# Optimization experiments

Hardware: AMD Instinct MI355X
Metric: run time of the kernel (lower is better)

The kernel has to match this reference:

```python
import jax, jax.numpy as jnp
import numpy as np
from jax import lax

EPS = 1e-5

# --- ApproxSign (ReActNet binary activation, STE with polynomial grad) ---
@jax.custom_vjp
def approx_sign(x):
    return jnp.sign(x)

def _as_fwd(x):
    return jnp.sign(x), x

def _as_bwd(x, g):
    # d/dx of piecewise-polynomial approx: 2-2|x| for |x|<1, else 0
    return (g * jnp.maximum(0.0, 2.0 - 2.0 * jnp.abs(x)),)

approx_sign.defvjp(_as_fwd, _as_bwd)


def rsign(x, bias):
    # learnable per-channel shift then binarize
    return approx_sign(x + bias[None, :, None, None])


def scaled_sign_weight(w):
    # per-output-channel scale * sign(w); straight-through identity grad to w
    scale = jnp.mean(jnp.abs(w), axis=(1, 2, 3), keepdims=True)
    bw = scale * jnp.sign(w)
    return lax.stop_gradient(bw - w) + w


def conv(x, w, stride, pad):
    return lax.conv_general_dilated(
        x, w, window_strides=(stride, stride), padding=[(pad, pad), (pad, pad)],
        dimension_numbers=("NCHW", "OIHW", "NCHW"))


def bn(x, g, b, m, v):
    inv = g / jnp.sqrt(v + EPS)
    return x * inv[None, :, None, None] + (b - m * inv)[None, :, None, None]


def rprelu(x, gamma, beta, zeta):
    t = x - gamma[None, :, None, None]
    return jnp.where(t > 0, t, beta[None, :, None, None] * t) + zeta[None, :, None, None]


def avgpool2(x):
    B, C, H, W = x.shape
    return x.reshape(B, C, H // 2, 2, W // 2, 2).mean(axis=(3, 5))


def setup_inputs() -> dict:
    key = jax.random.key(0)
    ks = jax.random.split(key, 16)
    C = 256
    d = {}
    d["x"] = jax.random.normal(ks[0], (64, C, 28, 28), dtype=jnp.float32)
    d["rsign_bias"] = jax.random.normal(ks[1], (C,), dtype=jnp.float32) * 0.1
    d["w1"] = jax.random.normal(ks[2], (C, C, 3, 3), dtype=jnp.float32) * 0.05
    d["bn1_g"] = jnp.ones((C,), jnp.float32)
    d["bn1_b"] = jnp.zeros((C,), jnp.float32)
    d["bn1_m"] = jax.random.normal(ks[3], (C,), dtype=jnp.float32) * 0.1
    d["bn1_v"] = jax.random.uniform(ks[4], (C,), dtype=jnp.float32, minval=0.5, maxval=1.5)
    d["w21"] = jax.random.normal(ks[5], (C, C, 1, 1), dtype=jnp.float32) * 0.05
    d["bn21_g"] = jnp.ones((C,), jnp.float32)
    d["bn21_b"] = jnp.zeros((C,), jnp.float32)
    d["bn21_m"] = jax.random.normal(ks[6], (C,), dtype=jnp.float32) * 0.1
    d["bn21_v"] = jax.random.uniform(ks[7], (C,), dtype=jnp.float32, minval=0.5, maxval=1.5)
    d["w22"] = jax.random.normal(ks[8], (C, C, 1, 1), dtype=jnp.float32) * 0.05
    d["bn22_g"] = jnp.ones((C,), jnp.float32)
    d["bn22_b"] = jnp.zeros((C,), jnp.float32)
    d["bn22_m"] = jax.random.normal(ks[9], (C,), dtype=jnp.float32) * 0.1
    d["bn22_v"] = jax.random.uniform(ks[10], (C,), dtype=jnp.float32, minval=0.5, maxval=1.5)
    d["pr_gamma"] = jax.random.normal(ks[11], (C,), dtype=jnp.float32) * 0.1
    d["pr_beta"] = jnp.full((C,), 0.25, jnp.float32)
    d["pr_zeta"] = jax.random.normal(ks[12], (C,), dtype=jnp.float32) * 0.1
    return d


def reference(x, rsign_bias, w1, bn1_g, bn1_b, bn1_m, bn1_v,
              w21, bn21_g, bn21_b, bn21_m, bn21_v,
              w22, bn22_g, bn22_b, bn22_m, bn22_v,
              pr_gamma, pr_beta, pr_zeta):
    # layer1: RSign -> 3x3 stride2 binary conv -> BN
    out = bn(conv(rsign(x, rsign_bias), scaled_sign_weight(w1), 2, 1),
             bn1_g, bn1_b, bn1_m, bn1_v)
    out1 = out + avgpool2(x)                       # residual with avgpooled input
    out2 = rprelu(out1, pr_gamma, pr_beta, pr_zeta)
    # two parallel 1x1 binary conv branches (shared RSign bias)
    a = rsign(out2, rsign_bias)
    out2_1 = bn(conv(a, scaled_sign_weight(w21), 1, 0), bn21_g, bn21_b, bn21_m, bn21_v)
    out2_2 = bn(conv(a, scaled_sign_weight(w22), 1, 0), bn22_g, bn22_b, bn22_m, bn22_v)
    out4_1 = rprelu(out2_1 + out2, pr_gamma, pr_beta, pr_zeta)
    out4_2 = rprelu(out2_2 + out2, pr_gamma, pr_beta, pr_zeta)
    return jnp.concatenate([out4_1, out4_2], axis=1)  # [B, 2C, H/2, W/2]
```

## Files before the change

kernel.cpp:

```cpp
#include <hip/hip_runtime.h>
#include <stdint.h>

#define EPS_BN 1e-5f

#define C 256
#define H 28
#define W 28
#define R196 196
#define M_TOT 12544
#define K1 2304

typedef __attribute__((ext_vector_type(4))) int   i32x4;
typedef __attribute__((ext_vector_type(4))) float f32x4;
typedef unsigned short ushort_t;
typedef unsigned int uint_t;

__device__ __forceinline__ char sgn_i8(float v) {
    return v > 0.f ? (char)1 : (v < 0.f ? (char)-1 : (char)0);
}
__device__ __forceinline__ uint_t sgn_b(float v) {
    return (uint_t)(unsigned char)sgn_i8(v);
}

__device__ __forceinline__ void gload16(const void* g, void* l) {
    __builtin_amdgcn_global_load_lds(
        (const __attribute__((address_space(1))) void*)g,
        (__attribute__((address_space(3))) void*)l, 16, 0, 0);
}


__global__ __launch_bounds__(256) void prep_sign(
    const float* __restrict__ w1,
    const float* __restrict__ bn1_g, const float* __restrict__ bn1_b,
    const float* __restrict__ bn1_m, const float* __restrict__ bn1_v,
    const float* __restrict__ w21,
    const float* __restrict__ bn21_g, const float* __restrict__ bn21_b,
    const float* __restrict__ bn21_m, const float* __restrict__ bn21_v,
    const float* __restrict__ w22,
    const float* __restrict__ bn22_g, const float* __restrict__ bn22_b,
    const float* __restrict__ bn22_m, const float* __restrict__ bn22_v,
    const float* __restrict__ x, const float* __restrict__ bias,
    char* __restrict__ bw1, char* __restrict__ bw2,
    float* __restrict__ alpha1, float* __restrict__ beta1,
    float* __restrict__ alpha2, float* __restrict__ beta2,
    char* __restrict__ a1p, float* __restrict__ pool)
{
    __shared__ uint_t lsign[1792];
    float* red = (float*)lsign;
    const int bid = blockIdx.x;
    const int t = threadIdx.x;

    if (bid < 768) {
        if (bid < 256) {
            const int oc = bid;
            const float* w = w1 + oc * K1;
            float s = 0.f;
            for (int i = t; i < K1; i += 256) s += fabsf(w[i]);
            red[t] = s; __syncthreads();
            for (int o = 128; o > 0; o >>= 1) {
                if (t < o) red[t] += red[t + o];
                __syncthreads();
            }
            const float scale = red[0] * (1.f / (float)K1);
            if (t == 0) {
                const float inv = bn1_g[oc] * rsqrtf(bn1_v[oc] + EPS_BN);
                alpha1[oc] = scale * inv;
                beta1[oc]  = bn1_b[oc] - bn1_m[oc] * inv;
            }
            const int ic = ((t & 3) << 6) | (t >> 2);
#pragma unroll
            for (int tap = 0; tap < 9; ++tap)
                bw1[oc * K1 + tap * 256 + t] = sgn_i8(w[ic * 9 + tap]);
        } else {
            const bool br2 = (bid >= 512);
            const int oc = (bid - 256) & 255;
            const float* w = (br2 ? w22 : w21) + oc * 256;
            red[t] = fabsf(w[t]); __syncthreads();
            for (int o = 128; o > 0; o >>= 1) {
                if (t < o) red[t] += red[t + o];
                __syncthreads();
            }
            const float scale = red[0] * (1.f / 256.f);
            const int n = oc + (br2 ? 256 : 0);
            if (t == 0) {
                const float g = br2 ? bn22_g[oc] : bn21_g[oc];
                const float b = br2 ? bn22_b[oc] : bn21_b[oc];
                const float m = br2 ? bn22_m[oc] : bn21_m[oc];
                const float v = br2 ? bn22_v[oc] : bn21_v[oc];
                const float inv = g * rsqrtf(v + EPS_BN);
                alpha2[n] = scale * inv;
                beta2[n]  = b - m * inv;
            }
            bw2[n * 256 + t] = sgn_i8(w[t]);
        }
        return;
    }

    const int sb = bid - 768;
    const int hh = sb & 1;
    const int bo = sb >> 1;
    const int b = bo / 14, oh = bo % 14;
    const float* xb = x + (size_t)(b * 256) * 784 + (2 * oh) * 28;

    for (int i = t; i < 896; i += 256) {
        const int lc = i / 7, q = i - lc * 7;
        const int c = 64 * (lc >> 5) + 32 * hh + (lc & 31);
        const float bc = bias[c];
        const float4 v0 = *(const float4*)(xb + c * 784 + 4 * q);
        const float4 v1 = *(const float4*)(xb + c * 784 + 28 + 4 * q);
        uint_t s0 = sgn_b(v0.x + bc) | (sgn_b(v0.y + bc) << 8) |
                    (sgn_b(v0.z + bc) << 16) | (sgn_b(v0.w + bc) << 24);
        uint_t s1 = sgn_b(v1.x + bc) | (sgn_b(v1.y + bc) << 8) |
                    (sgn_b(v1.z + bc) << 16) | (sgn_b(v1.w + bc) << 24);
        lsign[lc * 7 + q] = s0;
        lsign[896 + lc * 7 + q] = s1;
        float2 pr;
        pr.x = 0.25f * (v0.x + v0.y + v1.x + v1.y);
        pr.y = 0.25f * (v0.z + v0.w + v1.z + v1.w);
        *(float2*)(pool + (size_t)(b * 256 + c) * 196 + oh * 14 + 2 * q) = pr;
    }
    __syncthreads();

    for (int i = t; i < 448; i += 256) {
        const int tl = i & 31;
        const int q = (i >> 5) % 7;
        const int row = i / 224;
        const int tt = 32 * hh + tl;
        uint_t d[4];
#pragma unroll
        for (int e = 0; e < 4; ++e)
            d[e] = lsign[row * 896 + (tl + 32 * e) * 7 + q];
        char* orow = a1p + (size_t)((b * 30 + 2 * oh + row + 1) * 30) * 256;
#pragma unroll
        for (int j = 0; j < 4; ++j) {
            uint_t o = ((d[0] >> (8 * j)) & 0xffu)
                     | (((d[1] >> (8 * j)) & 0xffu) << 8)
                     | (((d[2] >> (8 * j)) & 0xffu) << 16)
                     | (((d[3] >> (8 * j)) & 0xffu) << 24);
            *(uint_t*)(orow + (4 * q + j + 1) * 256 + 4 * tt) = o;
        }
    }

    {
        char* orow0 = a1p + (size_t)((b * 30 + 2 * oh + 1) * 30) * 256;
        char* orow1 = a1p + (size_t)((b * 30 + 2 * oh + 2) * 30) * 256;
        const int bo2 = 128 * hh + (t & 127);
        if (t < 128) { orow0[bo2] = 0; orow1[bo2] = 0; }
        else         { orow0[29 * 256 + bo2] = 0; orow1[29 * 256 + bo2] = 0; }
    }
    if (oh == 0) {
        char* r0  = a1p + (size_t)(b * 900) * 256;
        char* r29 = a1p + (size_t)(b * 900 + 29 * 30) * 256;
        for (int idx = t; idx < 30 * 128; idx += 256) {
            const int colo = (idx >> 7) * 256 + 128 * hh + (idx & 127);
            r0[colo] = 0; r29[colo] = 0;
        }
    }
}

__global__ __launch_bounds__(512) void conv1_i8(
    const char* __restrict__ a1p,
    const char* __restrict__ bw1,
    const float* __restrict__ alpha1, const float* __restrict__ beta1,
    const float* __restrict__ p,
    const float* __restrict__ rsb,
    const float* __restrict__ prg, const float* __restrict__ prb,
    const float* __restrict__ prz,
    float* __restrict__ out2,
    char* __restrict__ a2)
{
    __shared__ char lA[2][64 * 128];
    __shared__ char lB[2][64 * 128];

    const int bid = blockIdx.x;
    const int wgid = (bid & 7) * 98 + (bid >> 3);
    const int mtile = wgid >> 2;
    const int ntile = wgid & 3;

    const int tid = threadIdx.x;
    const int wave = tid >> 6;
    const int lane = tid & 63;
    const int col = lane & 15;
    const int krow = lane >> 4;
    const int wr = wave >> 2;
    const int wc = wave & 3;
    const int l8 = lane >> 3;
    const int s8 = lane & 7;
    const int swz = ((s8 ^ l8) << 4);

    int pbA;
    {
        const int grow = wave * 8 + l8;
        const int m = mtile * 64 + grow;
        const int b = m / 196, r = m % 196;
        const int oh = r / 14, ow = r % 14;
        pbA = ((b * 30 + 2 * oh) * 30 + 2 * ow) * 256 + swz;
    }
    const int pbB = (ntile * 64 + wave * 8 + l8) * K1 + swz;

    int rswz[2];
#pragma unroll
    for (int ks = 0; ks < 2; ++ks)
        rswz[ks] = ((ks * 4 + krow) ^ (col & 7)) << 4;

    i32x4 acc[2] = {};

    auto stage = [&](int step, int buf) {
        const int tap = step >> 1;
        const int kc0 = (step & 1) << 7;
        const int kh = tap / 3, kw = tap - kh * 3;
        const int aoff = (kh * 30 + kw) * 256 + kc0;
        gload16(a1p + pbA + aoff, &lA[buf][0] + wave * 1024);
        gload16(bw1 + pbB + step * 128, &lB[buf][0] + wave * 1024);
    };

    stage(0, 0);

    int cur = 0;
    for (int step = 0; step < 18; ++step) {
        if (step + 1 < 18) {
            stage(step + 1, cur ^ 1);
            asm volatile("s_waitcnt vmcnt(2)" ::: "memory");
        } else {
            asm volatile("s_waitcnt vmcnt(0)" ::: "memory");
        }
        __builtin_amdgcn_s_barrier();
        __builtin_amdgcn_sched_barrier(0);

#pragma unroll
        for (int ks = 0; ks < 2; ++ks) {
            i32x4 bf[2], af;
#pragma unroll
            for (int im = 0; im < 2; ++im) {
                const int row = wr * 32 + im * 16 + col;
                bf[im] = *(const i32x4*)(&lA[cur][0] + row * 128 + rswz[ks]);
            }
            {
                const int row = wc * 16 + col;
                af = *(const i32x4*)(&lB[cur][0] + row * 128 + rswz[ks]);
            }
#pragma unroll
            for (int im = 0; im < 2; ++im)
                acc[im] = __builtin_amdgcn_mfma_i32_16x16x64_i8(
                    af, bf[im], acc[im], 0, 0, 0);
        }
        __builtin_amdgcn_sched_barrier(0);
        __builtin_amdgcn_s_barrier();
        cur ^= 1;
    }

#pragma unroll
    for (int im = 0; im < 2; ++im) {
        const int m = mtile * 64 + wr * 32 + im * 16 + col;
        const int b = m / 196, r = m % 196;
        const int n0 = ntile * 64 + wc * 16 + krow * 4;
        char spack[4];
#pragma unroll
        for (int j = 0; j < 4; ++j) {
            const int n = n0 + j;
            const int idx = (b * 256 + n) * 196 + r;
            float v = alpha1[n] * (float)acc[im][j] + beta1[n] + p[idx];
            const float t = v - prg[n];
            const float o = (t > 0.f ? t : prb[n] * t) + prz[n];
            out2[idx] = o;
            spack[j] = sgn_i8(o + rsb[n]);
        }
        *(char4*)(a2 + m * 256 + n0) = *(char4*)spack;
    }
}

__global__ __launch_bounds__(512) void conv1x1_i8(
    const char* __restrict__ a2,
    const char* __restrict__ bw2,
    const float* __restrict__ alpha2, const float* __restrict__ beta2,
    const float* __restrict__ out2,
    const float* __restrict__ prg, const float* __restrict__ prb,
    const float* __restrict__ prz,
    float* __restrict__ out)
{
    __shared__ char lA[2][64 * 128];
    __shared__ char lB[2][64 * 128];

    const int bid = blockIdx.x;
    const int wgid = (bid & 7) * 196 + (bid >> 3);
    const int mtile = wgid >> 3;
    const int ntile = wgid & 7;

    const int tid = threadIdx.x;
    const int wave = tid >> 6;
    const int lane = tid & 63;
    const int col = lane & 15;
    const int krow = lane >> 4;
    const int wr = wave >> 2;
    const int wc = wave & 3;
    const int l8 = lane >> 3;
    const int s8 = lane & 7;
    const int swz = ((s8 ^ l8) << 4);

    const int pbA = (mtile * 64 + wave * 8 + l8) * 256 + swz;
    const int pbB = (ntile * 64 + wave * 8 + l8) * 256 + swz;

#pragma unroll
    for (int h = 0; h < 2; ++h) {
        gload16(a2 + pbA + h * 128, &lA[h][0] + wave * 1024);
        gload16(bw2 + pbB + h * 128, &lB[h][0] + wave * 1024);
    }
    asm volatile("s_waitcnt vmcnt(0)" ::: "memory");
    __builtin_amdgcn_s_barrier();
    __builtin_amdgcn_sched_barrier(0);

    i32x4 acc[2] = {};
#pragma unroll
    for (int ks = 0; ks < 4; ++ks) {
        const int h = ks >> 1, k2 = ks & 1;
        const int ro = ((k2 * 4 + krow) ^ (col & 7)) << 4;
        i32x4 bf[2], af;
#pragma unroll
        for (int im = 0; im < 2; ++im) {
            const int row = wr * 32 + im * 16 + col;
            bf[im] = *(const i32x4*)(&lA[h][0] + row * 128 + ro);
        }
        {
            const int row = wc * 16 + col;
            af = *(const i32x4*)(&lB[h][0] + row * 128 + ro);
        }
#pragma unroll
        for (int im = 0; im < 2; ++im)
            acc[im] = __builtin_amdgcn_mfma_i32_16x16x64_i8(
                af, bf[im], acc[im], 0, 0, 0);
    }

#pragma unroll
    for (int im = 0; im < 2; ++im) {
        const int m = mtile * 64 + wr * 32 + im * 16 + col;
        const int b = m / 196, r = m % 196;
#pragma unroll
        for (int j = 0; j < 4; ++j) {
            const int n = ntile * 64 + wc * 16 + krow * 4 + j;
            const int oc = n & 255;
            float v = alpha2[n] * (float)acc[im][j] + beta2[n]
                    + out2[(b * 256 + oc) * 196 + r];
            const float t = v - prg[oc];
            out[(size_t)(b * 512 + n) * 196 + r] =
                (t > 0.f ? t : prb[oc] * t) + prz[oc];
        }
    }
}

extern "C" void kernel_launch(void* const* d_in, const int* in_sizes, int n_in,
                              void* d_out, int out_size, void* d_ws, size_t ws_size,
                              hipStream_t stream)
{
    (void)in_sizes; (void)n_in; (void)out_size; (void)ws_size;

    const float* x         = (const float*)d_in[0];
    const float* rsign_b   = (const float*)d_in[1];
    const float* w1        = (const float*)d_in[2];
    const float* bn1_g     = (const float*)d_in[3];
    const float* bn1_b     = (const float*)d_in[4];
    const float* bn1_m     = (const float*)d_in[5];
    const float* bn1_v     = (const float*)d_in[6];
    const float* w21       = (const float*)d_in[7];
    const float* bn21_g    = (const float*)d_in[8];
    const float* bn21_b    = (const float*)d_in[9];
    const float* bn21_m    = (const float*)d_in[10];
    const float* bn21_v    = (const float*)d_in[11];
    const float* w22       = (const float*)d_in[12];
    const float* bn22_g    = (const float*)d_in[13];
    const float* bn22_b    = (const float*)d_in[14];
    const float* bn22_m    = (const float*)d_in[15];
    const float* bn22_v    = (const float*)d_in[16];
    const float* pr_gamma  = (const float*)d_in[17];
    const float* pr_beta   = (const float*)d_in[18];
    const float* pr_zeta   = (const float*)d_in[19];

    char* ws = (char*)d_ws;
    size_t off = 0;
    char* a1p     = (char*)(ws + off);  off += (size_t)14745600;
    char* bw1     = (char*)(ws + off);  off += (size_t)589824;
    char* bw2     = (char*)(ws + off);  off += (size_t)131072;
    float* pool   = (float*)(ws + off); off += (size_t)3211264 * 4;
    float* out2   = (float*)(ws + off); off += (size_t)3211264 * 4;
    char* a2      = (char*)(ws + off);  off += (size_t)3211264;
    float* alpha1 = (float*)(ws + off); off += 1024;
    float* beta1  = (float*)(ws + off); off += 1024;
    float* alpha2 = (float*)(ws + off); off += 2048;
    float* beta2  = (float*)(ws + off); off += 2048;

    prep_sign<<<2560, 256, 0, stream>>>(
        w1, bn1_g, bn1_b, bn1_m, bn1_v,
        w21, bn21_g, bn21_b, bn21_m, bn21_v,
        w22, bn22_g, bn22_b, bn22_m, bn22_v,
        x, rsign_b,
        bw1, bw2, alpha1, beta1, alpha2, beta2, a1p, pool);

    conv1_i8<<<784, 512, 0, stream>>>(
        a1p, bw1, alpha1, beta1, pool, rsign_b,
        pr_gamma, pr_beta, pr_zeta, out2, a2);

    conv1x1_i8<<<1568, 512, 0, stream>>>(
        a2, bw2, alpha2, beta2, out2,
        pr_gamma, pr_beta, pr_zeta, (float*)d_out);
}
```

Measured before the change: 60.92 us.

## Enlarge conv workgroup tiles to 128x128 with 1024-thread blocks

Both int8 MFMA conv kernels move from 64x64 to 128x128 output tiles, using 16 waves per block. Each wave now computes a 2x2 set of 16x16 MFMA tiles instead of 2x1, and the LDS buffers double in size. The XCD-aware block remapping is replaced by a plain mtile/ntile split. The goal is more operand reuse and fewer global loads per output. The cost is fewer blocks (196 and 392) on a GPU with many CUs, which risks leaving CUs idle, plus higher LDS and register use per block.

```diff
diff --git a/kernel.cpp b/kernel.cpp
--- a/kernel.cpp
+++ b/kernel.cpp
@@ -158,7 +158,7 @@
     }
 }
 
-__global__ __launch_bounds__(512) void conv1_i8(
+__global__ __launch_bounds__(1024) void conv1_i8(
     const char* __restrict__ a1p,
     const char* __restrict__ bw1,
     const float* __restrict__ alpha1, const float* __restrict__ beta1,
@@ -169,13 +169,12 @@
     float* __restrict__ out2,
     char* __restrict__ a2)
 {
-    __shared__ char lA[2][64 * 128];
-    __shared__ char lB[2][64 * 128];
+    __shared__ char lA[2][128 * 128];
+    __shared__ char lB[2][128 * 128];
 
     const int bid = blockIdx.x;
-    const int wgid = (bid & 7) * 98 + (bid >> 3);
-    const int mtile = wgid >> 2;
-    const int ntile = wgid & 3;
+    const int mtile = bid >> 1;
+    const int ntile = bid & 1;
 
     const int tid = threadIdx.x;
     const int wave = tid >> 6;
@@ -191,19 +190,19 @@
     int pbA;
     {
         const int grow = wave * 8 + l8;
-        const int m = mtile * 64 + grow;
+        const int m = mtile * 128 + grow;
         const int b = m / 196, r = m % 196;
         const int oh = r / 14, ow = r % 14;
         pbA = ((b * 30 + 2 * oh) * 30 + 2 * ow) * 256 + swz;
     }
-    const int pbB = (ntile * 64 + wave * 8 + l8) * K1 + swz;
+    const int pbB = (ntile * 128 + wave * 8 + l8) * K1 + swz;
 
     int rswz[2];
 #pragma unroll
     for (int ks = 0; ks < 2; ++ks)
         rswz[ks] = ((ks * 4 + krow) ^ (col & 7)) << 4;
 
-    i32x4 acc[2] = {};
+    i32x4 acc[2][2] = {};
 
     auto stage = [&](int step, int buf) {
         const int tap = step >> 1;
@@ -229,20 +228,23 @@
 
 #pragma unroll
         for (int ks = 0; ks < 2; ++ks) {
-            i32x4 bf[2], af;
+            i32x4 bf[2], af[2];
 #pragma unroll
             for (int im = 0; im < 2; ++im) {
                 const int row = wr * 32 + im * 16 + col;
                 bf[im] = *(const i32x4*)(&lA[cur][0] + row * 128 + rswz[ks]);
             }
-            {
-                const int row = wc * 16 + col;
-                af = *(const i32x4*)(&lB[cur][0] + row * 128 + rswz[ks]);
+#pragma unroll
+            for (int in = 0; in < 2; ++in) {
+                const int row = wc * 32 + in * 16 + col;
+                af[in] = *(const i32x4*)(&lB[cur][0] + row * 128 + rswz[ks]);
             }
 #pragma unroll
             for (int im = 0; im < 2; ++im)
-                acc[im] = __builtin_amdgcn_mfma_i32_16x16x64_i8(
-                    af, bf[im], acc[im], 0, 0, 0);
+#pragma unroll
+                for (int in = 0; in < 2; ++in)
+                    acc[im][in] = __builtin_amdgcn_mfma_i32_16x16x64_i8(
+                        af[in], bf[im], acc[im][in], 0, 0, 0);
         }
         __builtin_amdgcn_sched_barrier(0);
         __builtin_amdgcn_s_barrier();
@@ -251,25 +253,28 @@
 
 #pragma unroll
     for (int im = 0; im < 2; ++im) {
-        const int m = mtile * 64 + wr * 32 + im * 16 + col;
+        const int m = mtile * 128 + wr * 32 + im * 16 + col;
         const int b = m / 196, r = m % 196;
-        const int n0 = ntile * 64 + wc * 16 + krow * 4;
-        char spack[4];
-#pragma unroll
-        for (int j = 0; j < 4; ++j) {
-            const int n = n0 + j;
-            const int idx = (b * 256 + n) * 196 + r;
-            float v = alpha1[n] * (float)acc[im][j] + beta1[n] + p[idx];
-            const float t = v - prg[n];
-            const float o = (t > 0.f ? t : prb[n] * t) + prz[n];
-            out2[idx] = o;
-            spack[j] = sgn_i8(o + rsb[n]);
-        }
-        *(char4*)(a2 + m * 256 + n0) = *(char4*)spack;
-    }
-}
-
-__global__ __launch_bounds__(512) void conv1x1_i8(
+#pragma unroll
+        for (int in = 0; in < 2; ++in) {
+            const int n0 = ntile * 128 + wc * 32 + in * 16 + krow * 4;
+            char spack[4];
+#pragma unroll
+            for (int j = 0; j < 4; ++j) {
+                const int n = n0 + j;
+                const int idx = (b * 256 + n) * 196 + r;
+                float v = alpha1[n] * (float)acc[im][in][j] + beta1[n] + p[idx];
+                const float t = v - prg[n];
+                const float o = (t > 0.f ? t : prb[n] * t) + prz[n];
+                out2[idx] = o;
+                spack[j] = sgn_i8(o + rsb[n]);
+            }
+            *(char4*)(a2 + m * 256 + n0) = *(char4*)spack;
+        }
+    }
+}
+
+__global__ __launch_bounds__(1024) void conv1x1_i8(
     const char* __restrict__ a2,
     const char* __restrict__ bw2,
     const float* __restrict__ alpha2, const float* __restrict__ beta2,
@@ -278,13 +283,12 @@
     const float* __restrict__ prz,
     float* __restrict__ out)
 {
-    __shared__ char lA[2][64 * 128];
-    __shared__ char lB[2][64 * 128];
+    __shared__ char lA[2][128 * 128];
+    __shared__ char lB[2][128 * 128];
 
     const int bid = blockIdx.x;
-    const int wgid = (bid & 7) * 196 + (bid >> 3);
-    const int mtile = wgid >> 3;
-    const int ntile = wgid & 7;
+    const int mtile = bid >> 2;
+    const int ntile = bid & 3;
 
     const int tid = threadIdx.x;
     const int wave = tid >> 6;
@@ -297,8 +301,8 @@
     const int s8 = lane & 7;
     const int swz = ((s8 ^ l8) << 4);
 
-    const int pbA = (mtile * 64 + wave * 8 + l8) * 256 + swz;
-    const int pbB = (ntile * 64 + wave * 8 + l8) * 256 + swz;
+    const int pbA = (mtile * 128 + wave * 8 + l8) * 256 + swz;
+    const int pbB = (ntile * 128 + wave * 8 + l8) * 256 + swz;
 
 #pragma unroll
     for (int h = 0; h < 2; ++h) {
@@ -309,40 +313,46 @@
     __builtin_amdgcn_s_barrier();
     __builtin_amdgcn_sched_barrier(0);
 
-    i32x4 acc[2] = {};
+    i32x4 acc[2][2] = {};
 #pragma unroll
     for (int ks = 0; ks < 4; ++ks) {
         const int h = ks >> 1, k2 = ks & 1;
         const int ro = ((k2 * 4 + krow) ^ (col & 7)) << 4;
-        i32x4 bf[2], af;
+        i32x4 bf[2], af[2];
 #pragma unroll
         for (int im = 0; im < 2; ++im) {
             const int row = wr * 32 + im * 16 + col;
             bf[im] = *(const i32x4*)(&lA[h][0] + row * 128 + ro);
         }
-        {
-            const int row = wc * 16 + col;
-            af = *(const i32x4*)(&lB[h][0] + row * 128 + ro);
+#pragma unroll
+        for (int in = 0; in < 2; ++in) {
+            const int row = wc * 32 + in * 16 + col;
+            af[in] = *(const i32x4*)(&lB[h][0] + row * 128 + ro);
         }
 #pragma unroll
         for (int im = 0; im < 2; ++im)
-            acc[im] = __builtin_amdgcn_mfma_i32_16x16x64_i8(
-                af, bf[im], acc[im], 0, 0, 0);
+#pragma unroll
+            for (int in = 0; in < 2; ++in)
+                acc[im][in] = __builtin_amdgcn_mfma_i32_16x16x64_i8(
+                    af[in], bf[im], acc[im][in], 0, 0, 0);
     }
 
 #pragma unroll
     for (int im = 0; im < 2; ++im) {
-        const int m = mtile * 64 + wr * 32 + im * 16 + col;
+        const int m = mtile * 128 + wr * 32 + im * 16 + col;
         const int b = m / 196, r = m % 196;
 #pragma unroll
-        for (int j = 0; j < 4; ++j) {
-            const int n = ntile * 64 + wc * 16 + krow * 4 + j;
-            const int oc = n & 255;
-            float v = alpha2[n] * (float)acc[im][j] + beta2[n]
-                    + out2[(b * 256 + oc) * 196 + r];
-            const float t = v - prg[oc];
-            out[(size_t)(b * 512 + n) * 196 + r] =
-                (t > 0.f ? t : prb[oc] * t) + prz[oc];
+        for (int in = 0; in < 2; ++in) {
+#pragma unroll
+            for (int j = 0; j < 4; ++j) {
+                const int n = ntile * 128 + wc * 32 + in * 16 + krow * 4 + j;
+                const int oc = n & 255;
+                float v = alpha2[n] * (float)acc[im][in][j] + beta2[n]
+                        + out2[(b * 256 + oc) * 196 + r];
+                const float t = v - prg[oc];
+                out[(size_t)(b * 512 + n) * 196 + r] =
+                    (t > 0.f ? t : prb[oc] * t) + prz[oc];
+            }
         }
     }
 }
@@ -394,11 +404,11 @@
         x, rsign_b,
         bw1, bw2, alpha1, beta1, alpha2, beta2, a1p, pool);
 
-    conv1_i8<<<784, 512, 0, stream>>>(
+    conv1_i8<<<196, 1024, 0, stream>>>(
         a1p, bw1, alpha1, beta1, pool, rsign_b,
         pr_gamma, pr_beta, pr_zeta, out2, a2);
 
-    conv1x1_i8<<<1568, 512, 0, stream>>>(
+    conv1x1_i8<<<392, 1024, 0, stream>>>(
         a2, bw2, alpha2, beta2, out2,
         pr_gamma, pr_beta, pr_zeta, (float*)d_out);
 }
```

After: 76.22 us. +25.1%, slower.
